# Kernel optimization log

Measured on AMD Instinct MI355X. Metric: run time of the kernel, lower is better.

The kernel has to match this reference:

```python
import jax, jax.numpy as jnp
import numpy as np

# ---- model constants (from init_kwargs) ----
HIDDEN = 4096
NUM_HEADS = 32
HEAD_DIM = HIDDEN // NUM_HEADS  # 128
ROPE_THETA = 10000.0
P8 = 512
P6 = 1024
P4 = HIDDEN - P8 - P6  # 2560
BLOCK = 32  # scale-factor block size (SFB* are sized out*p//32)


def _block_quant(x, bits):
    """Symmetric per-32-element-block fake quantization along the last dim.
    Emulates the dequantized math of the packed 4/6/8-bit tiers in mixedgemm."""
    qmax = 2.0 ** (bits - 1) - 1.0
    shp = x.shape
    xb = x.reshape(shp[:-1] + (shp[-1] // BLOCK, BLOCK))
    scale = jnp.maximum(jnp.max(jnp.abs(xb), axis=-1, keepdims=True) / qmax, 1e-8)
    dq = (jnp.clip(jnp.round(xb / scale), -qmax, qmax) * scale).reshape(shp)
    return dq


def _mixed_quant(x):
    """Split reordered features into [p4 | p6 | p8] tiers and quantize each."""
    xn, xs, xo = jnp.split(x, [P4, P4 + P6], axis=-1)
    return jnp.concatenate([_block_quant(xn, 4), _block_quant(xs, 6), _block_quant(xo, 8)], axis=-1)


def _qlinear(x, W, reorder_index):
    """reorder_quantize_x + mixedgemm.matmul (dequantized reference math).
    x: [T, in], W: [out, in] (stored already in reordered column order)."""
    xq = _mixed_quant(x[..., reorder_index])
    Wq = _mixed_quant(W)
    return xq @ Wq.T


def _rotate_half(x):
    h = x.shape[-1] // 2
    return jnp.concatenate([-x[..., h:], x[..., :h]], axis=-1)


def setup_inputs() -> dict:
    key = jax.random.key(0)
    k1, k2, k3, k4, k5 = jax.random.split(key, 5)
    B, S = 2, 2048
    hidden_states = jax.random.normal(k1, (B, S, HIDDEN), dtype=jnp.float32)
    Wq = jax.random.normal(k2, (HIDDEN, HIDDEN), dtype=jnp.float32) * 0.02
    Wk = jax.random.normal(k3, (HIDDEN, HIDDEN), dtype=jnp.float32) * 0.02
    Wv = jax.random.normal(k4, (HIDDEN, HIDDEN), dtype=jnp.float32) * 0.02
    Wo = jax.random.normal(k5, (HIDDEN, HIDDEN), dtype=jnp.float32) * 0.02
    position_ids = jnp.broadcast_to(jnp.arange(S, dtype=jnp.int32)[None, :], (B, S))
    reorder_index = jnp.arange(HIDDEN, dtype=jnp.int32)  # default identity reorder
    return {"hidden_states": hidden_states, "Wq": Wq, "Wk": Wk, "Wv": Wv,
            "Wo": Wo, "position_ids": position_ids, "reorder_index": reorder_index}


def reference(hidden_states, Wq, Wk, Wv, Wo, position_ids, reorder_index):
    B, S, H = hidden_states.shape
    x2 = hidden_states.reshape(B * S, H)

    q = _qlinear(x2, Wq, reorder_index).reshape(B, S, NUM_HEADS, HEAD_DIM)
    k = _qlinear(x2, Wk, reorder_index).reshape(B, S, NUM_HEADS, HEAD_DIM)
    v = _qlinear(x2, Wv, reorder_index).reshape(B, S, NUM_HEADS, HEAD_DIM)

    # LlamaRotaryEmbedding: cos/sin [B, S, head_dim], unsqueeze_dim=2 (broadcast over heads)
    inv_freq = 1.0 / (ROPE_THETA ** (jnp.arange(0, HEAD_DIM, 2, dtype=jnp.float32) / HEAD_DIM))
    freqs = position_ids.astype(jnp.float32)[..., None] * inv_freq  # [B, S, hd/2]
    emb = jnp.concatenate([freqs, freqs], axis=-1)                  # [B, S, hd]
    cos = jnp.cos(emb)[:, :, None, :]
    sin = jnp.sin(emb)[:, :, None, :]
    q = q * cos + _rotate_half(q) * sin
    k = k * cos + _rotate_half(k) * sin

    # causal SDPA over [B, nH, S, hd]
    qh = q.transpose(0, 2, 1, 3)
    kh = k.transpose(0, 2, 1, 3)
    vh = v.transpose(0, 2, 1, 3)
    scaling = 1.0 / jnp.sqrt(jnp.float32(HEAD_DIM))
    scores = jnp.einsum('bhqd,bhkd->bhqk', qh, kh) * scaling
    causal = jnp.tril(jnp.ones((S, S), dtype=bool))
    scores = jnp.where(causal[None, None], scores, jnp.finfo(scores.dtype).min)
    probs = jax.nn.softmax(scores, axis=-1)
    attn = jnp.einsum('bhqk,bhkd->bhqd', probs, vh)  # [B, nH, S, hd]

    attn = attn.transpose(0, 2, 1, 3).reshape(B * S, H)
    out = _qlinear(attn, Wo, reorder_index).reshape(B, S, H)
    return out
```

## Files before the change

### kernel.cpp

```cpp
#include <hip/hip_runtime.h>


typedef __bf16 bf16_t;
typedef __bf16 bf16x8 __attribute__((ext_vector_type(8)));
typedef float f32x4 __attribute__((ext_vector_type(4)));

#define MFMA16(a, b, c) __builtin_amdgcn_mfma_f32_16x16x32_bf16(a, b, c, 0, 0, 0)

__device__ __forceinline__ void split_bf16(float x, bf16_t& h, bf16_t& l) {
    h = (bf16_t)x;
    l = (bf16_t)(x - (float)h);
}

typedef const __attribute__((address_space(1))) void glb_v;
typedef __attribute__((address_space(3))) void lds_v;

__device__ __forceinline__ void gl_lds16(const void* g, void* l) {
    __builtin_amdgcn_global_load_lds((glb_v*)g, (lds_v*)l, 16, 0, 0);
}

template<int OUT_I8>
__global__ void quant_is(const float* __restrict__ srcf,
                         const bf16_t* __restrict__ shi, const bf16_t* __restrict__ slo,
                         const int* __restrict__ rid, int src_split, int gather,
                         signed char* __restrict__ qi8, bf16_t* __restrict__ qbf,
                         float* __restrict__ qs) {
    long idx = (long)blockIdx.x * 256 + threadIdx.x;
    int col = (int)(idx & 4095);
    long row = idx >> 12;
    int g = gather ? rid[col] : col;
    long si = row * 4096 + g;
    float v = src_split ? ((float)shi[si] + (float)slo[si]) : srcf[si];
    float a = fabsf(v);
#pragma unroll
    for (int off = 1; off < 32; off <<= 1) a = fmaxf(a, __shfl_xor(a, off, 32));
    float qmax = (col < 2560) ? 7.0f : (col < 3584 ? 31.0f : 127.0f);
    float scale = fmaxf(a / qmax, 1e-8f);
    float q = rintf(v * (1.0f / scale));
    q = fminf(fmaxf(q, -qmax), qmax);
    if (OUT_I8) qi8[idx] = (signed char)q;
    else        qbf[idx] = (bf16_t)q;
    if ((col & 31) == 0) qs[row * 128 + (col >> 5)] = scale;
}

template<int OSPL>
__global__ __launch_bounds__(256, 2) void gemm_is(
    const signed char* __restrict__ Ai, const float* __restrict__ As,
    const bf16_t* __restrict__ Bi, const float* __restrict__ Bs,
    bf16_t* __restrict__ OHi, bf16_t* __restrict__ OLo, float* __restrict__ Of) {
    constexpr int K = 4096, N = 4096;
    __shared__ __align__(16) bf16_t sA[128 * 32];
    __shared__ __align__(16) bf16_t sB[128 * 32];
    __shared__ float sAs[128];
    __shared__ float sBs[128];

    const int tid = threadIdx.x;
    const int bx = blockIdx.x & 31, by = blockIdx.x >> 5;
    const int rowBase = by << 7, colBase = bx << 7;
    const int lane = tid & 63, wave = tid >> 6;
    const int wr = (wave >> 1) << 6, wc = (wave & 1) << 6;
    const int n16 = lane & 15, quad = lane >> 4;

    f32x4 acc[4][4];
#pragma unroll
    for (int m = 0; m < 4; ++m)
#pragma unroll
        for (int n = 0; n < 4; ++n) acc[m][n] = (f32x4){0.f, 0.f, 0.f, 0.f};

    const int ar = tid >> 1, acb = (tid & 1) << 4;
    const int br = tid >> 2, bcb = (tid & 3) << 3;

    for (int kb = 0; kb < 128; ++kb) {
        const int k0 = kb << 5;
        __syncthreads();
        gl_lds16(&Bi[(long)(colBase + br) * K + k0 + bcb], &sB[(long)tid << 3]);
        gl_lds16(&Bi[(long)(colBase + 64 + br) * K + k0 + bcb], &sB[(long)(256 + tid) << 3]);
        {
            int4 raw = *(const int4*)&Ai[(long)(rowBase + ar) * K + k0 + acb];
            const signed char* pc = (const signed char*)&raw;
            bf16x8 v0, v1;
#pragma unroll
            for (int j = 0; j < 8; ++j) {
                v0[j] = (bf16_t)(float)pc[j];
                v1[j] = (bf16_t)(float)pc[8 + j];
            }
            *(bf16x8*)&sA[(ar << 5) + acb] = v0;
            *(bf16x8*)&sA[(ar << 5) + acb + 8] = v1;
        }
        if (tid < 128) sAs[tid] = As[(long)(rowBase + tid) * 128 + kb];
        else           sBs[tid - 128] = Bs[(long)(colBase + tid - 128) * 128 + kb];
        __syncthreads();

        bf16x8 a[4], b[4];
        f32x4 asv[4];
        float bsv[4];
#pragma unroll
        for (int m = 0; m < 4; ++m) {
            a[m] = *(const bf16x8*)&sA[((wr + (m << 4) + n16) << 5) + (quad << 3)];
            asv[m] = *(const f32x4*)&sAs[wr + (m << 4) + (quad << 2)];
        }
#pragma unroll
        for (int n = 0; n < 4; ++n) {
            b[n] = *(const bf16x8*)&sB[((wc + (n << 4) + n16) << 5) + (quad << 3)];
            bsv[n] = sBs[wc + (n << 4) + n16];
        }
        const f32x4 z = (f32x4){0.f, 0.f, 0.f, 0.f};
#pragma unroll
        for (int m = 0; m < 4; ++m)
#pragma unroll
            for (int n = 0; n < 4; ++n) {
                f32x4 sc = MFMA16(a[m], b[n], z);
                float bn = bsv[n];
#pragma unroll
                for (int r = 0; r < 4; ++r)
                    acc[m][n][r] = fmaf(asv[m][r] * bn, sc[r], acc[m][n][r]);
            }
    }

#pragma unroll
    for (int m = 0; m < 4; ++m)
#pragma unroll
        for (int n = 0; n < 4; ++n) {
            int row = rowBase + wr + (m << 4) + (quad << 2);
            int col = colBase + wc + (n << 4) + n16;
#pragma unroll
            for (int r = 0; r < 4; ++r) {
                if (OSPL) {
                    bf16_t h, l;
                    split_bf16(acc[m][n][r], h, l);
                    OHi[(long)(row + r) * N + col] = h;
                    OLo[(long)(row + r) * N + col] = l;
                } else {
                    Of[(long)(row + r) * N + col] = acc[m][n][r];
                }
            }
        }
}

__global__ void rope2(bf16_t* __restrict__ qh, bf16_t* __restrict__ ql,
                      bf16_t* __restrict__ kh, bf16_t* __restrict__ kl,
                      const int* __restrict__ pos) {
    int t = blockIdx.x;
    int tid = threadIdx.x;
    __shared__ float cs[64], sn[64];
    if (tid < 64) {
        float invf = (float)pow(10000.0, -(double)tid / 64.0);
        float ang = (float)pos[t] * invf;
        cs[tid] = (float)cos((double)ang);
        sn[tid] = (float)sin((double)ang);
    }
    __syncthreads();
#pragma unroll
    for (int i = 0; i < 8; ++i) {
        int l = i * 256 + tid;
        int hh = l >> 6, d = l & 63;
        long base = (long)t * 4096 + hh * 128 + d;
        float c = cs[d], s = sn[d];
        float a0 = (float)qh[base] + (float)ql[base];
        float a1 = (float)qh[base + 64] + (float)ql[base + 64];
        float r0 = a0 * c - a1 * s, r1 = a1 * c + a0 * s;
        bf16_t x, y;
        split_bf16(r0, x, y); qh[base] = x;      ql[base] = y;
        split_bf16(r1, x, y); qh[base + 64] = x; ql[base + 64] = y;
        float b0 = (float)kh[base] + (float)kl[base];
        float b1 = (float)kh[base + 64] + (float)kl[base + 64];
        r0 = b0 * c - b1 * s; r1 = b1 * c + b0 * s;
        split_bf16(r0, x, y); kh[base] = x;      kl[base] = y;
        split_bf16(r1, x, y); kh[base + 64] = x; kl[base + 64] = y;
    }
}

__global__ void transpose_vt(const ushort* __restrict__ vh, const ushort* __restrict__ vl,
                             ushort* __restrict__ th, ushort* __restrict__ tl) {
    __shared__ ushort t0[64][68];
    __shared__ ushort t1[64][68];
    int ct = blockIdx.x, tt = blockIdx.y, tid = threadIdx.x;
#pragma unroll
    for (int i = 0; i < 16; ++i) {
        int l = i * 256 + tid, r = l >> 6, c = l & 63;
        long idx = (long)(tt * 64 + r) * 4096 + ct * 64 + c;
        t0[r][c] = vh[idx];
        t1[r][c] = vl[idx];
    }
    __syncthreads();
#pragma unroll
    for (int i = 0; i < 16; ++i) {
        int l = i * 256 + tid, dr = l >> 6, sc = l & 63;
        int colg = ct * 64 + dr, hh = colg >> 7, dl = colg & 127;
        int tok = tt * 64 + sc, b = tok >> 11, s = tok & 2047;
        long o = (long)((b * 32 + hh) * 128 + dl) * 2048 + s;
        th[o] = t0[sc][dr];
        tl[o] = t1[sc][dr];
    }
}

__global__ __launch_bounds__(256, 2) void flash_attn3(
    const bf16_t* __restrict__ qhp, const bf16_t* __restrict__ qlp,
    const bf16_t* __restrict__ khp, const bf16_t* __restrict__ klp,
    const bf16_t* __restrict__ vth, const bf16_t* __restrict__ vtl,
    bf16_t* __restrict__ ohi, bf16_t* __restrict__ olo) {
    __shared__ __align__(16) char smem[75776];

    const int bid = blockIdx.x;
    const int xcd = bid & 7, ixd = bid >> 3;
    const int bh = (xcd << 3) + (ixd >> 4);
    const int qt = 15 - (ixd & 15);
    const int b = bh >> 5, h = bh & 31;
    const int tid = threadIdx.x;
    const int wave = tid >> 6, lane = tid & 63;
    const int n16 = lane & 15, quad = lane >> 4;
    const long tokB = (long)b * 2048;
    const int q0 = qt * 128 + wave * 32;
    const float scale = 0.08838834764831845f;

    bf16_t (*pH)[40] = (bf16_t (*)[40])(smem + 65536 + wave * 2560);
    bf16_t (*pL)[40] = (bf16_t (*)[40])(smem + 65536 + wave * 2560 + 1280);

    bf16x8 qhF[2][4], qlF[2][4];
#pragma unroll
    for (int m = 0; m < 2; ++m) {
        long qoff = (tokB + q0 + m * 16 + n16) * 4096 + h * 128 + quad * 8;
#pragma unroll
        for (int f = 0; f < 4; ++f) {
            qhF[m][f] = *(const bf16x8*)&qhp[qoff + f * 32];
            qlF[m][f] = *(const bf16x8*)&qlp[qoff + f * 32];
        }
    }

    const int kr0 = wave * 8 + quad;
    const int kc0 = ((((lane & 15) << 4) ^ (quad << 4)) >> 1);
    const int kc1 = ((((lane & 15) << 4) ^ ((4 + quad) << 4)) >> 1);
    const int kd0 = kr0 * 256 + ((lane & 15) << 4);
    const int vr0 = wave * 32 + (lane >> 2);
    const int vc0 = ((((lane & 3) << 4) ^ (((lane >> 2) & 3) << 4)) >> 1);
    const int vd0 = vr0 * 64 + ((lane & 3) << 4);
    const long vrow_g = (long)(bh * 128 + vr0) * 2048;

#define STAGE(BUF, KB) do {                                                   \
    char* _bb = smem + ((BUF) << 15);                                         \
    const long _kt = tokB + (long)(KB) * 32;                                  \
    const long _g0 = (_kt + kr0) * 4096 + h * 128;                            \
    gl_lds16(khp + _g0 + kc0,           _bb + kd0);                           \
    gl_lds16(klp + _g0 + kc0,           _bb + 8192 + kd0);                    \
    gl_lds16(khp + _g0 + 4 * 4096 + kc1, _bb + 1024 + kd0);                   \
    gl_lds16(klp + _g0 + 4 * 4096 + kc1, _bb + 8192 + 1024 + kd0);            \
    const long _v0 = vrow_g + (KB) * 32 + vc0;                                \
    gl_lds16(vth + _v0,                 _bb + 16384 + vd0);                   \
    gl_lds16(vtl + _v0,                 _bb + 24576 + vd0);                   \
    gl_lds16(vth + _v0 + 16 * 2048,     _bb + 16384 + 1024 + vd0);            \
    gl_lds16(vtl + _v0 + 16 * 2048,     _bb + 24576 + 1024 + vd0);            \
} while (0)

    f32x4 o[2][8];
#pragma unroll
    for (int m = 0; m < 2; ++m)
#pragma unroll
        for (int dc = 0; dc < 8; ++dc) o[m][dc] = (f32x4){0.f, 0.f, 0.f, 0.f};
    float m_i[2][4], l_i[2][4];
#pragma unroll
    for (int m = 0; m < 2; ++m)
#pragma unroll
        for (int r = 0; r < 4; ++r) { m_i[m][r] = -1e30f; l_i[m][r] = 0.f; }

    const int nkb = 4 * qt + 4;
    const int lastkb = 4 * qt + wave;

    STAGE(0, 0);
    asm volatile("s_waitcnt vmcnt(0)" ::: "memory");
    __builtin_amdgcn_s_barrier();
    asm volatile("" ::: "memory");

    for (int kb = 0; kb < nkb; ++kb) {
        if (kb + 1 < nkb) STAGE((kb + 1) & 1, kb + 1);

        if (kb <= lastkb) {
            const char* bK = smem + ((kb & 1) << 15);
            const char* bV = bK + 16384;

            f32x4 s[2][2];
            const int rswz = (n16 & 7) << 4;
#pragma unroll
            for (int nt = 0; nt < 2; ++nt) {
                const int krow = nt * 16 + n16;
                bf16x8 kh[4], kl[4];
#pragma unroll
                for (int f = 0; f < 4; ++f) {
                    const int cb = ((f << 6) | (quad << 4)) ^ rswz;
                    kh[f] = *(const bf16x8*)(bK + krow * 256 + cb);
                    kl[f] = *(const bf16x8*)(bK + 8192 + krow * 256 + cb);
                }
#pragma unroll
                for (int m = 0; m < 2; ++m) {
                    f32x4 sc = (f32x4){0.f, 0.f, 0.f, 0.f};
#pragma unroll
                    for (int f = 0; f < 4; ++f) {
                        sc = MFMA16(qhF[m][f], kh[f], sc);
                        sc = MFMA16(qhF[m][f], kl[f], sc);
                        sc = MFMA16(qlF[m][f], kh[f], sc);
                    }
                    s[m][nt] = sc;
                }
            }

            if (kb == lastkb) {
                const int key0 = kb * 32 + n16;
#pragma unroll
                for (int m = 0; m < 2; ++m)
#pragma unroll
                    for (int nt = 0; nt < 2; ++nt)
#pragma unroll
                        for (int r = 0; r < 4; ++r) {
                            int qrow = q0 + m * 16 + quad * 4 + r;
                            s[m][nt][r] = (key0 + nt * 16 <= qrow) ? s[m][nt][r] * scale
                                                                   : -1e30f;
                        }
            } else {
#pragma unroll
                for (int m = 0; m < 2; ++m)
#pragma unroll
                    for (int nt = 0; nt < 2; ++nt)
#pragma unroll
                        for (int r = 0; r < 4; ++r) s[m][nt][r] *= scale;
            }

            float alpha[2][4];
#pragma unroll
            for (int m = 0; m < 2; ++m)
#pragma unroll
                for (int r = 0; r < 4; ++r) {
                    float mx = fmaxf(s[m][0][r], s[m][1][r]);
#pragma unroll
                    for (int off = 1; off < 16; off <<= 1) mx = fmaxf(mx, __shfl_xor(mx, off, 64));
                    float mnew = fmaxf(m_i[m][r], mx);
                    alpha[m][r] = expf(m_i[m][r] - mnew);
                    m_i[m][r] = mnew;
                    float p0 = expf(s[m][0][r] - mnew);
                    float p1 = expf(s[m][1][r] - mnew);
                    s[m][0][r] = p0;
                    s[m][1][r] = p1;
                    float sum = p0 + p1;
#pragma unroll
                    for (int off = 1; off < 16; off <<= 1) sum += __shfl_xor(sum, off, 64);
                    l_i[m][r] = l_i[m][r] * alpha[m][r] + sum;
                }

            bf16x8 ph2[2], pl2[2];
#pragma unroll
            for (int m = 0; m < 2; ++m) {
#pragma unroll
                for (int nt = 0; nt < 2; ++nt)
#pragma unroll
                    for (int r = 0; r < 4; ++r) {
                        bf16_t hh2, ll2;
                        split_bf16(s[m][nt][r], hh2, ll2);
                        pH[quad * 4 + r][nt * 16 + n16] = hh2;
                        pL[quad * 4 + r][nt * 16 + n16] = ll2;
                    }
                ph2[m] = *(const bf16x8*)&pH[n16][quad * 8];
                pl2[m] = *(const bf16x8*)&pL[n16][quad * 8];
            }

#pragma unroll
            for (int dc = 0; dc < 8; ++dc) {
                const int vrow = dc * 16 + n16;
                const int vcb = ((quad ^ (n16 & 3)) << 4);
                bf16x8 vh = *(const bf16x8*)(bV + vrow * 64 + vcb);
                bf16x8 vl = *(const bf16x8*)(bV + 8192 + vrow * 64 + vcb);
#pragma unroll
                for (int m = 0; m < 2; ++m) {
#pragma unroll
                    for (int r = 0; r < 4; ++r) o[m][dc][r] *= alpha[m][r];
                    o[m][dc] = MFMA16(ph2[m], vh, o[m][dc]);
                    o[m][dc] = MFMA16(ph2[m], vl, o[m][dc]);
                    o[m][dc] = MFMA16(pl2[m], vh, o[m][dc]);
                }
            }
        }

        asm volatile("s_waitcnt vmcnt(0)" ::: "memory");
        __builtin_amdgcn_s_barrier();
        asm volatile("" ::: "memory");
    }
#undef STAGE

#pragma unroll
    for (int m = 0; m < 2; ++m)
#pragma unroll
        for (int r = 0; r < 4; ++r) {
            float invl = 1.0f / l_i[m][r];
            long row = tokB + q0 + m * 16 + quad * 4 + r;
#pragma unroll
            for (int dc = 0; dc < 8; ++dc) {
                bf16_t hh2, ll2;
                split_bf16(o[m][dc][r] * invl, hh2, ll2);
                ohi[row * 4096 + h * 128 + dc * 16 + n16] = hh2;
                olo[row * 4096 + h * 128 + dc * 16 + n16] = ll2;
            }
        }
}

extern "C" void kernel_launch(void* const* d_in, const int* in_sizes, int n_in,
                              void* d_out, int out_size, void* d_ws, size_t ws_size,
                              hipStream_t stream) {
    const float* x  = (const float*)d_in[0];
    const float* Wq = (const float*)d_in[1];
    const float* Wk = (const float*)d_in[2];
    const float* Wv = (const float*)d_in[3];
    const float* Wo = (const float*)d_in[4];
    const int* pos  = (const int*)d_in[5];
    const int* rid  = (const int*)d_in[6];

    const size_t MB = 1024ull * 1024ull;
    char* ws = (char*)d_ws;
    bf16_t* QH = (bf16_t*)(ws);
    bf16_t* QL = (bf16_t*)(ws + 32 * MB);
    bf16_t* KH = (bf16_t*)(ws + 64 * MB);
    bf16_t* KL = (bf16_t*)(ws + 96 * MB);
    char* S = ws + 128 * MB;
    signed char* Xi = (signed char*)S;
    float*  Xs  = (float*)(S + 16 * MB);
    bf16_t* Wi  = (bf16_t*)(S + 18 * MB);
    float*  Wsc = (float*)(S + 50 * MB);
    bf16_t* VTh = (bf16_t*)S;
    bf16_t* VTl = (bf16_t*)(S + 32 * MB);
    bf16_t* OUh = (bf16_t*)d_out;
    bf16_t* OUl = (bf16_t*)((char*)d_out + 32 * MB);

    const int QG = 65536;

    quant_is<1><<<QG, 256, 0, stream>>>(x, nullptr, nullptr, rid, 0, 1, Xi, nullptr, Xs);

    quant_is<0><<<QG, 256, 0, stream>>>(Wq, nullptr, nullptr, rid, 0, 0, nullptr, Wi, Wsc);
    gemm_is<1><<<1024, 256, 0, stream>>>(Xi, Xs, Wi, Wsc, QH, QL, nullptr);
    quant_is<0><<<QG, 256, 0, stream>>>(Wk, nullptr, nullptr, rid, 0, 0, nullptr, Wi, Wsc);
    gemm_is<1><<<1024, 256, 0, stream>>>(Xi, Xs, Wi, Wsc, KH, KL, nullptr);
    quant_is<0><<<QG, 256, 0, stream>>>(Wv, nullptr, nullptr, rid, 0, 0, nullptr, Wi, Wsc);
    gemm_is<1><<<1024, 256, 0, stream>>>(Xi, Xs, Wi, Wsc, OUh, OUl, nullptr);

    rope2<<<4096, 256, 0, stream>>>(QH, QL, KH, KL, pos);

    transpose_vt<<<dim3(64, 64), 256, 0, stream>>>((const ushort*)OUh, (const ushort*)OUl,
                                                   (ushort*)VTh, (ushort*)VTl);

    flash_attn3<<<1024, 256, 0, stream>>>(QH, QL, KH, KL, VTh, VTl, OUh, OUl);

    quant_is<1><<<QG, 256, 0, stream>>>(nullptr, OUh, OUl, rid, 1, 1, Xi, nullptr, Xs);
    quant_is<0><<<QG, 256, 0, stream>>>(Wo, nullptr, nullptr, rid, 0, 0, nullptr, Wi, Wsc);
    gemm_is<0><<<1024, 256, 0, stream>>>(Xi, Xs, Wi, Wsc, nullptr, nullptr, (float*)d_out);

    (void)in_sizes; (void)n_in; (void)out_size; (void)ws_size;
}
```

Before: 2.533 ms.

## Double-buffer quantized GEMM, transpose scale layout, vectorize quantization, swizzle blocks per XCD

The quantized GEMM now double-buffers its A, B and scale tiles in LDS. It issues the next k-block's global loads, including the scales, before computing on the current tile, which should hide load latency and leaves one barrier per iteration. Scales are stored transposed (k-block major) so each k-step can fetch them with contiguous 4-byte LDS-direct loads. The quant kernel handles 4 elements per thread with packed stores, and GEMM blocks are remapped so neighbouring column tiles share an XCD for better L2 reuse. Workspace buffers are reassigned to fit the transposed layouts, and the LDS footprint doubles, which could reduce occupancy.

Measured after the change: 2.381 ms. 6.0% less time.

```diff
diff --git a/kernel.cpp b/kernel.cpp
--- a/kernel.cpp
+++ b/kernel.cpp
@@ -2,6 +2,7 @@
 
 
 typedef __bf16 bf16_t;
+typedef __bf16 bf16x4 __attribute__((ext_vector_type(4)));
 typedef __bf16 bf16x8 __attribute__((ext_vector_type(8)));
 typedef float f32x4 __attribute__((ext_vector_type(4)));
 
@@ -17,6 +18,9 @@
 
 __device__ __forceinline__ void gl_lds16(const void* g, void* l) {
     __builtin_amdgcn_global_load_lds((glb_v*)g, (lds_v*)l, 16, 0, 0);
+}
+__device__ __forceinline__ void gl_lds4(const void* g, void* l) {
+    __builtin_amdgcn_global_load_lds((glb_v*)g, (lds_v*)l, 4, 0, 0);
 }
 
 template<int OUT_I8>
@@ -24,85 +28,130 @@
                          const bf16_t* __restrict__ shi, const bf16_t* __restrict__ slo,
                          const int* __restrict__ rid, int src_split, int gather,
                          signed char* __restrict__ qi8, bf16_t* __restrict__ qbf,
-                         float* __restrict__ qs) {
-    long idx = (long)blockIdx.x * 256 + threadIdx.x;
+                         float* __restrict__ qsT) {
+    long idx = ((long)blockIdx.x * 256 + threadIdx.x) << 2;
     int col = (int)(idx & 4095);
-    long row = idx >> 12;
-    int g = gather ? rid[col] : col;
-    long si = row * 4096 + g;
-    float v = src_split ? ((float)shi[si] + (float)slo[si]) : srcf[si];
-    float a = fabsf(v);
-#pragma unroll
-    for (int off = 1; off < 32; off <<= 1) a = fmaxf(a, __shfl_xor(a, off, 32));
+    long rowoff = idx & ~4095L;
+    float v[4];
+    float a = 0.f;
+#pragma unroll
+    for (int j = 0; j < 4; ++j) {
+        int g = gather ? rid[col + j] : col + j;
+        float x = src_split ? ((float)shi[rowoff + g] + (float)slo[rowoff + g])
+                            : srcf[rowoff + g];
+        v[j] = x;
+        a = fmaxf(a, fabsf(x));
+    }
+#pragma unroll
+    for (int off = 1; off < 8; off <<= 1) a = fmaxf(a, __shfl_xor(a, off, 64));
     float qmax = (col < 2560) ? 7.0f : (col < 3584 ? 31.0f : 127.0f);
     float scale = fmaxf(a / qmax, 1e-8f);
-    float q = rintf(v * (1.0f / scale));
-    q = fminf(fmaxf(q, -qmax), qmax);
-    if (OUT_I8) qi8[idx] = (signed char)q;
-    else        qbf[idx] = (bf16_t)q;
-    if ((col & 31) == 0) qs[row * 128 + (col >> 5)] = scale;
+    float inv = 1.0f / scale;
+    if (OUT_I8) {
+        int pk = 0;
+#pragma unroll
+        for (int j = 0; j < 4; ++j) {
+            float q = fminf(fmaxf(rintf(v[j] * inv), -qmax), qmax);
+            pk |= (int)(unsigned char)(signed char)(int)q << (8 * j);
+        }
+        *(int*)&qi8[idx] = pk;
+    } else {
+        bf16x4 pk;
+#pragma unroll
+        for (int j = 0; j < 4; ++j) {
+            float q = fminf(fmaxf(rintf(v[j] * inv), -qmax), qmax);
+            pk[j] = (bf16_t)q;
+        }
+        *(bf16x4*)&qbf[idx] = pk;
+    }
+    if ((col & 31) == 0) qsT[((long)(col >> 5) << 12) + (idx >> 12)] = scale;
 }
 
 template<int OSPL>
 __global__ __launch_bounds__(256, 2) void gemm_is(
-    const signed char* __restrict__ Ai, const float* __restrict__ As,
-    const bf16_t* __restrict__ Bi, const float* __restrict__ Bs,
+    const signed char* __restrict__ Ai, const float* __restrict__ AsT,
+    const bf16_t* __restrict__ Bi, const float* __restrict__ BsT,
     bf16_t* __restrict__ OHi, bf16_t* __restrict__ OLo, float* __restrict__ Of) {
     constexpr int K = 4096, N = 4096;
-    __shared__ __align__(16) bf16_t sA[128 * 32];
-    __shared__ __align__(16) bf16_t sB[128 * 32];
-    __shared__ float sAs[128];
-    __shared__ float sBs[128];
+    __shared__ __align__(16) bf16_t sA[2][128 * 32];
+    __shared__ __align__(16) bf16_t sB[2][128 * 32];
+    __shared__ __align__(16) float  sS[2][256];
 
     const int tid = threadIdx.x;
-    const int bx = blockIdx.x & 31, by = blockIdx.x >> 5;
+    const int bid = blockIdx.x;
+    const int xcd = bid & 7, j = bid >> 3;
+    const int bx = xcd * 4 + (j & 3), by = j >> 2;
     const int rowBase = by << 7, colBase = bx << 7;
     const int lane = tid & 63, wave = tid >> 6;
     const int wr = (wave >> 1) << 6, wc = (wave & 1) << 6;
     const int n16 = lane & 15, quad = lane >> 4;
 
+    const int arow = tid >> 1, achk = (tid & 1) << 4;
+    const long aSrc = (long)(rowBase + arow) * K + achk;
+    const int aDst = arow * 64 + achk * 2;
+    const int brow = tid >> 2, bchk = (tid & 3) << 3;
+    const long bSrc0 = (long)(colBase + brow) * K + bchk;
+    const long bSrc1 = (long)(colBase + 64 + brow) * K + bchk;
+    const int bDst = tid << 4;
+    const int sIsB = wave >> 1;
+    const float* sPtr = (sIsB ? BsT + colBase : AsT + rowBase) + ((wave & 1) << 6) + lane;
+    const int sDst = (sIsB ? 512 : 0) + ((wave & 1) << 8) + (lane << 2);
+
     f32x4 acc[4][4];
 #pragma unroll
     for (int m = 0; m < 4; ++m)
 #pragma unroll
         for (int n = 0; n < 4; ++n) acc[m][n] = (f32x4){0.f, 0.f, 0.f, 0.f};
 
-    const int ar = tid >> 1, acb = (tid & 1) << 4;
-    const int br = tid >> 2, bcb = (tid & 3) << 3;
+    int4 aReg;
+
+#define ISSUE(BUF, KB) do {                                                   \
+    char* _b = (char*)sB[BUF]; char* _s = (char*)sS[BUF];                     \
+    const int _k0 = (KB) << 5;                                                \
+    gl_lds16(Bi + bSrc0 + _k0, _b + bDst);                                    \
+    gl_lds16(Bi + bSrc1 + _k0, _b + 4096 + bDst);                             \
+    gl_lds4(sPtr + ((long)(KB) << 12), _s + sDst);                            \
+    aReg = *(const int4*)(Ai + aSrc + _k0);                                   \
+} while (0)
+
+#define FINISH(BUF) do {                                                      \
+    asm volatile("s_waitcnt vmcnt(0)" ::: "memory");                          \
+    const signed char* _pc = (const signed char*)&aReg;                       \
+    bf16x8 _v0, _v1;                                                          \
+    _Pragma("unroll")                                                         \
+    for (int _j = 0; _j < 8; ++_j) {                                          \
+        _v0[_j] = (bf16_t)(float)_pc[_j];                                     \
+        _v1[_j] = (bf16_t)(float)_pc[8 + _j];                                 \
+    }                                                                         \
+    *(bf16x8*)((char*)sA[BUF] + aDst) = _v0;                                  \
+    *(bf16x8*)((char*)sA[BUF] + aDst + 16) = _v1;                             \
+    asm volatile("s_waitcnt lgkmcnt(0)" ::: "memory");                        \
+    __builtin_amdgcn_s_barrier();                                             \
+    asm volatile("" ::: "memory");                                            \
+} while (0)
+
+    ISSUE(0, 0);
+    FINISH(0);
 
     for (int kb = 0; kb < 128; ++kb) {
-        const int k0 = kb << 5;
-        __syncthreads();
-        gl_lds16(&Bi[(long)(colBase + br) * K + k0 + bcb], &sB[(long)tid << 3]);
-        gl_lds16(&Bi[(long)(colBase + 64 + br) * K + k0 + bcb], &sB[(long)(256 + tid) << 3]);
-        {
-            int4 raw = *(const int4*)&Ai[(long)(rowBase + ar) * K + k0 + acb];
-            const signed char* pc = (const signed char*)&raw;
-            bf16x8 v0, v1;
-#pragma unroll
-            for (int j = 0; j < 8; ++j) {
-                v0[j] = (bf16_t)(float)pc[j];
-                v1[j] = (bf16_t)(float)pc[8 + j];
-            }
-            *(bf16x8*)&sA[(ar << 5) + acb] = v0;
-            *(bf16x8*)&sA[(ar << 5) + acb + 8] = v1;
-        }
-        if (tid < 128) sAs[tid] = As[(long)(rowBase + tid) * 128 + kb];
-        else           sBs[tid - 128] = Bs[(long)(colBase + tid - 128) * 128 + kb];
-        __syncthreads();
-
+        const int cur = kb & 1;
+        if (kb < 127) ISSUE(cur ^ 1, kb + 1);
+
+        const char* pA = (const char*)sA[cur];
+        const char* pB = (const char*)sB[cur];
+        const char* pS = (const char*)sS[cur];
         bf16x8 a[4], b[4];
         f32x4 asv[4];
         float bsv[4];
 #pragma unroll
         for (int m = 0; m < 4; ++m) {
-            a[m] = *(const bf16x8*)&sA[((wr + (m << 4) + n16) << 5) + (quad << 3)];
-            asv[m] = *(const f32x4*)&sAs[wr + (m << 4) + (quad << 2)];
+            a[m] = *(const bf16x8*)(pA + (wr + (m << 4) + n16) * 64 + (quad << 4));
+            asv[m] = *(const f32x4*)(pS + ((wr + (m << 4) + (quad << 2)) << 2));
         }
 #pragma unroll
         for (int n = 0; n < 4; ++n) {
-            b[n] = *(const bf16x8*)&sB[((wc + (n << 4) + n16) << 5) + (quad << 3)];
-            bsv[n] = sBs[wc + (n << 4) + n16];
+            b[n] = *(const bf16x8*)(pB + (wc + (n << 4) + n16) * 64 + (quad << 4));
+            bsv[n] = *(const float*)(pS + 512 + ((wc + (n << 4) + n16) << 2));
         }
         const f32x4 z = (f32x4){0.f, 0.f, 0.f, 0.f};
 #pragma unroll
@@ -115,7 +164,11 @@
                 for (int r = 0; r < 4; ++r)
                     acc[m][n][r] = fmaf(asv[m][r] * bn, sc[r], acc[m][n][r]);
             }
-    }
+
+        if (kb < 127) FINISH(cur ^ 1);
+    }
+#undef ISSUE
+#undef FINISH
 
 #pragma unroll
     for (int m = 0; m < 4; ++m)
@@ -416,26 +469,29 @@
     bf16_t* QL = (bf16_t*)(ws + 32 * MB);
     bf16_t* KH = (bf16_t*)(ws + 64 * MB);
     bf16_t* KL = (bf16_t*)(ws + 96 * MB);
-    char* S = ws + 128 * MB;
-    signed char* Xi = (signed char*)S;
-    float*  Xs  = (float*)(S + 16 * MB);
-    bf16_t* Wi  = (bf16_t*)(S + 18 * MB);
-    float*  Wsc = (float*)(S + 50 * MB);
-    bf16_t* VTh = (bf16_t*)S;
-    bf16_t* VTl = (bf16_t*)(S + 32 * MB);
+    signed char* Xi = (signed char*)(ws + 128 * MB);
+    float*  XsT = (float*)(ws + 144 * MB);
+    float*  WsT = (float*)(ws + 146 * MB);
+    bf16_t* Wi  = (bf16_t*)(ws + 160 * MB);
+    bf16_t* VTh = (bf16_t*)(ws + 128 * MB);
+    bf16_t* VTl = (bf16_t*)(ws + 160 * MB);
+    signed char* Xi2 = (signed char*)(ws + 64 * MB);
+    float*  Xs2T = (float*)(ws + 96 * MB);
+    bf16_t* Wo_i = (bf16_t*)(ws + 128 * MB);
+    float*  WoST = (float*)(ws + 160 * MB);
     bf16_t* OUh = (bf16_t*)d_out;
     bf16_t* OUl = (bf16_t*)((char*)d_out + 32 * MB);
 
-    const int QG = 65536;
-
-    quant_is<1><<<QG, 256, 0, stream>>>(x, nullptr, nullptr, rid, 0, 1, Xi, nullptr, Xs);
-
-    quant_is<0><<<QG, 256, 0, stream>>>(Wq, nullptr, nullptr, rid, 0, 0, nullptr, Wi, Wsc);
-    gemm_is<1><<<1024, 256, 0, stream>>>(Xi, Xs, Wi, Wsc, QH, QL, nullptr);
-    quant_is<0><<<QG, 256, 0, stream>>>(Wk, nullptr, nullptr, rid, 0, 0, nullptr, Wi, Wsc);
-    gemm_is<1><<<1024, 256, 0, stream>>>(Xi, Xs, Wi, Wsc, KH, KL, nullptr);
-    quant_is<0><<<QG, 256, 0, stream>>>(Wv, nullptr, nullptr, rid, 0, 0, nullptr, Wi, Wsc);
-    gemm_is<1><<<1024, 256, 0, stream>>>(Xi, Xs, Wi, Wsc, OUh, OUl, nullptr);
+    const int QG = 16384;
+
+    quant_is<1><<<QG, 256, 0, stream>>>(x, nullptr, nullptr, rid, 0, 1, Xi, nullptr, XsT);
+
+    quant_is<0><<<QG, 256, 0, stream>>>(Wq, nullptr, nullptr, rid, 0, 0, nullptr, Wi, WsT);
+    gemm_is<1><<<1024, 256, 0, stream>>>(Xi, XsT, Wi, WsT, QH, QL, nullptr);
+    quant_is<0><<<QG, 256, 0, stream>>>(Wk, nullptr, nullptr, rid, 0, 0, nullptr, Wi, WsT);
+    gemm_is<1><<<1024, 256, 0, stream>>>(Xi, XsT, Wi, WsT, KH, KL, nullptr);
+    quant_is<0><<<QG, 256, 0, stream>>>(Wv, nullptr, nullptr, rid, 0, 0, nullptr, Wi, WsT);
+    gemm_is<1><<<1024, 256, 0, stream>>>(Xi, XsT, Wi, WsT, OUh, OUl, nullptr);
 
     rope2<<<4096, 256, 0, stream>>>(QH, QL, KH, KL, pos);
 
@@ -444,9 +500,9 @@
 
     flash_attn3<<<1024, 256, 0, stream>>>(QH, QL, KH, KL, VTh, VTl, OUh, OUl);
 
-    quant_is<1><<<QG, 256, 0, stream>>>(nullptr, OUh, OUl, rid, 1, 1, Xi, nullptr, Xs);
-    quant_is<0><<<QG, 256, 0, stream>>>(Wo, nullptr, nullptr, rid, 0, 0, nullptr, Wi, Wsc);
-    gemm_is<0><<<1024, 256, 0, stream>>>(Xi, Xs, Wi, Wsc, nullptr, nullptr, (float*)d_out);
+    quant_is<1><<<QG, 256, 0, stream>>>(nullptr, OUh, OUl, rid, 1, 1, Xi2, nullptr, Xs2T);
+    quant_is<0><<<QG, 256, 0, stream>>>(Wo, nullptr, nullptr, rid, 0, 0, nullptr, Wo_i, WoST);
+    gemm_is<0><<<1024, 256, 0, stream>>>(Xi2, Xs2T, Wo_i, WoST, nullptr, nullptr, (float*)d_out);
 
     (void)in_sizes; (void)n_in; (void)out_size; (void)ws_size;
 }
```
